# Kernel tuning notes

Measured on AMD Instinct MI355X. Metric: run time of the kernel, lower is better.

## Reference

```python
import jax, jax.numpy as jnp
import numpy as np

B, T, D, H, DH = 2, 2048, 1024, 16, 64
LN_EPS = 1e-5


def setup_inputs() -> dict:
    key = jax.random.key(0)
    ks = jax.random.split(key, 16)
    s = 0.02
    return {
        "query_sequences": jax.random.normal(ks[0], (B, T, D), jnp.float32),
        "key_sequences": jax.random.normal(ks[1], (B, T, D), jnp.float32),
        "value_sequences": jax.random.normal(ks[2], (B, T, D), jnp.float32),
        "key_value_sequence_lengths": jax.random.randint(ks[3], (B,), 1, T + 1),
        "Wq": jax.random.normal(ks[4], (D, H * DH), jnp.float32) * s,
        "bq": jnp.zeros((H * DH,), jnp.float32),
        "Wk": jax.random.normal(ks[5], (D, H * DH), jnp.float32) * s,
        "bk": jnp.zeros((H * DH,), jnp.float32),
        "Wv": jax.random.normal(ks[6], (D, H * DH), jnp.float32) * s,
        "bv": jnp.zeros((H * DH,), jnp.float32),
        "Wo": jax.random.normal(ks[7], (H * DH, D), jnp.float32) * s,
        "bo": jnp.zeros((D,), jnp.float32),
        "gamma": jnp.ones((D,), jnp.float32),
        "beta": jnp.zeros((D,), jnp.float32),
    }


def _layer_norm(x, gamma, beta):
    mu = jnp.mean(x, axis=-1, keepdims=True)
    var = jnp.var(x, axis=-1, keepdims=True)
    return (x - mu) * jax.lax.rsqrt(var + LN_EPS) * gamma + beta


def reference(query_sequences, key_sequences, value_sequences,
              key_value_sequence_lengths, Wq, bq, Wk, bk, Wv, bv, Wo, bo,
              gamma, beta):
    # pre-LN (self-attn: same LN applied to q, k, v inputs)
    q_in = _layer_norm(query_sequences, gamma, beta)
    k_in = _layer_norm(key_sequences, gamma, beta)
    v_in = _layer_norm(value_sequences, gamma, beta)

    # projections -> [B, H, T, DH]
    q = (q_in @ Wq + bq).reshape(B, T, H, DH).transpose(0, 2, 1, 3)
    k = (k_in @ Wk + bk).reshape(B, T, H, DH).transpose(0, 2, 1, 3)
    v = (v_in @ Wv + bv).reshape(B, T, H, DH).transpose(0, 2, 1, 3)

    scale = 1.0 / jnp.sqrt(jnp.float32(DH))
    scores = jnp.einsum('bhtd,bhTd->bhtT', q, k) * scale  # [B,H,Tq,Tk]

    # key padding mask: key position < sequence length
    pad_mask = jnp.arange(T)[None, None, None, :] < key_value_sequence_lengths[:, None, None, None]
    # causal mask (self_attn and in_decoder)
    causal = jnp.tril(jnp.ones((T, T), bool))[None, None]
    mask = pad_mask & causal
    scores = jnp.where(mask, scores, -jnp.inf)

    attn = jax.nn.softmax(scores, axis=-1)  # dropout=0 (eval)
    attn_viz = attn.reshape(B * H, T, T)

    out = jnp.einsum('bhtT,bhTd->bhtd', attn, v)
    out = out.transpose(0, 2, 1, 3).reshape(B, T, H * DH)
    out = out @ Wo + bo
    return out, attn_viz
```

## Files before the change

kernel.cpp:

```cpp
#include <hip/hip_runtime.h>
#include <hip/hip_bf16.h>

#define B_  2
#define T_  2048
#define D_  1024
#define H_  16
#define DH_ 64
#define M_  (B_*T_)

typedef __bf16 bf16;
typedef __bf16 bf16x8 __attribute__((ext_vector_type(8)));
typedef __bf16 bf16x4 __attribute__((ext_vector_type(4)));
typedef float  f32x4  __attribute__((ext_vector_type(4)));

__global__ __launch_bounds__(256) void ln_kernel(
    const float* __restrict__ xq, const float* __restrict__ xk,
    const float* __restrict__ xv, const float* __restrict__ gamma,
    const float* __restrict__ beta,
    bf16* __restrict__ oq, bf16* __restrict__ ok, bf16* __restrict__ ov)
{
    const int row = blockIdx.x;
    const int sel = blockIdx.y;
    const float* x = (sel == 0 ? xq : sel == 1 ? xk : xv) + (size_t)row * D_;
    bf16*        o = (sel == 0 ? oq : sel == 1 ? ok : ov) + (size_t)row * D_;
    const int tid = threadIdx.x;

    float4 v = *(const float4*)&x[tid * 4];
    float s  = v.x + v.y + v.z + v.w;
    float s2 = v.x*v.x + v.y*v.y + v.z*v.z + v.w*v.w;
    for (int off = 32; off > 0; off >>= 1) {
        s  += __shfl_down(s,  off, 64);
        s2 += __shfl_down(s2, off, 64);
    }
    __shared__ float red[8];
    const int wave = tid >> 6, lane = tid & 63;
    if (lane == 0) { red[wave] = s; red[4 + wave] = s2; }
    __syncthreads();
    s  = red[0] + red[1] + red[2] + red[3];
    s2 = red[4] + red[5] + red[6] + red[7];
    const float mu   = s * (1.0f / D_);
    const float var  = s2 * (1.0f / D_) - mu * mu;
    const float rstd = rsqrtf(var + 1e-5f);

    float4 g  = *(const float4*)&gamma[tid * 4];
    float4 bb = *(const float4*)&beta[tid * 4];
    bf16x4 o4;
    o4[0] = (bf16)((v.x - mu) * rstd * g.x + bb.x);
    o4[1] = (bf16)((v.y - mu) * rstd * g.y + bb.y);
    o4[2] = (bf16)((v.z - mu) * rstd * g.z + bb.z);
    o4[3] = (bf16)((v.w - mu) * rstd * g.w + bb.w);
    *(bf16x4*)&o[tid * 4] = o4;
}

__global__ __launch_bounds__(256) void wconv_kernel(
    const float* __restrict__ Wq, const float* __restrict__ Wk,
    const float* __restrict__ Wv, const float* __restrict__ Wo,
    bf16* __restrict__ wqt, bf16* __restrict__ wkt,
    bf16* __restrict__ wvt, bf16* __restrict__ wot)
{
    const float* Ws[4] = {Wq, Wk, Wv, Wo};
    bf16*        Wt[4] = {wqt, wkt, wvt, wot};
    const float* W = Ws[blockIdx.z];
    bf16*        O = Wt[blockIdx.z];
    const int n0 = blockIdx.x * 32, k0 = blockIdx.y * 32;
    __shared__ float tile[32][33];
    const int tid = threadIdx.x;
    #pragma unroll
    for (int i = 0; i < 4; i++) {
        int e = tid + i * 256;
        int r = e >> 5, c = e & 31;
        tile[r][c] = W[(size_t)(k0 + r) * 1024 + n0 + c];
    }
    __syncthreads();
    #pragma unroll
    for (int i = 0; i < 4; i++) {
        int e = tid + i * 256;
        int nr = e >> 5, kc = e & 31;
        O[(size_t)(n0 + nr) * 1024 + k0 + kc] = (bf16)tile[kc][nr];
    }
}

template <int MODE>
__global__ __launch_bounds__(256) void gemm_bt(
    const bf16* __restrict__ A, const bf16* __restrict__ Bt,
    const float* __restrict__ bias, void* __restrict__ Cout)
{
    __shared__ bf16 sA[128][40];
    __shared__ bf16 sB[128][40];
    const int tid  = threadIdx.x;
    const int wave = tid >> 6, lane = tid & 63;
    const int quad = lane >> 4, l16 = lane & 15;
    const int wr = (wave >> 1) * 64, wc = (wave & 1) * 64;
    const int m0 = blockIdx.y * 128, n0 = blockIdx.x * 128;

    f32x4 acc[4][4] = {};
    const int r0   = tid >> 2;
    const int r1   = 64 + (tid >> 2);
    const int off0 = (tid & 3) * 8;

    for (int k0 = 0; k0 < 1024; k0 += 32) {
        __syncthreads();
        *(bf16x8*)&sA[r0][off0] = *(const bf16x8*)&A[(size_t)(m0 + r0) * 1024 + k0 + off0];
        *(bf16x8*)&sA[r1][off0] = *(const bf16x8*)&A[(size_t)(m0 + r1) * 1024 + k0 + off0];
        *(bf16x8*)&sB[r0][off0] = *(const bf16x8*)&Bt[(size_t)(n0 + r0) * 1024 + k0 + off0];
        *(bf16x8*)&sB[r1][off0] = *(const bf16x8*)&Bt[(size_t)(n0 + r1) * 1024 + k0 + off0];
        __syncthreads();

        bf16x8 af[4], bfr[4];
        #pragma unroll
        for (int i = 0; i < 4; i++) af[i]  = *(bf16x8*)&sA[wr + i * 16 + l16][quad * 8];
        #pragma unroll
        for (int j = 0; j < 4; j++) bfr[j] = *(bf16x8*)&sB[wc + j * 16 + l16][quad * 8];
        #pragma unroll
        for (int i = 0; i < 4; i++)
            #pragma unroll
            for (int j = 0; j < 4; j++)
                acc[i][j] = __builtin_amdgcn_mfma_f32_16x16x32_bf16(af[i], bfr[j], acc[i][j], 0, 0, 0);
    }

    #pragma unroll
    for (int i = 0; i < 4; i++) {
        #pragma unroll
        for (int j = 0; j < 4; j++) {
            const int n = n0 + wc + j * 16 + l16;
            const float bia = bias[n];
            #pragma unroll
            for (int r = 0; r < 4; r++) {
                const int m = m0 + wr + i * 16 + quad * 4 + r;
                const float v = acc[i][j][r] + bia;
                if (MODE == 0) {
                    const int b = m >> 11, t = m & 2047, h = n >> 6, dh = n & 63;
                    ((bf16*)Cout)[(((size_t)b * H_ + h) * T_ + t) * DH_ + dh] = (bf16)v;
                } else {
                    ((float*)Cout)[(size_t)m * 1024 + n] = v;
                }
            }
        }
    }
}

__global__ __launch_bounds__(256) void attn_kernel(
    const bf16* __restrict__ Qh, const bf16* __restrict__ Kh,
    const bf16* __restrict__ Vh, const int* __restrict__ lens,
    float* __restrict__ attn_out, bf16* __restrict__ Obuf)
{
    const int bh = blockIdx.y;
    const int b = bh >> 4, h = bh & 15;
    const int bx = blockIdx.x;
    const int q0 = bx * 64;
    const int len = lens[b];
    const bf16* Qp = Qh + (size_t)bh * T_ * DH_;
    const bf16* Kp = Kh + (size_t)bh * T_ * DH_;
    const bf16* Vp = Vh + (size_t)bh * T_ * DH_;
    float* attnp = attn_out + (size_t)bh * T_ * T_;

    const int tid  = threadIdx.x;
    const int wave = tid >> 6, lane = tid & 63;
    const int quad = lane >> 4, l16 = lane & 15;
    const float scale = 0.125f;

    __shared__ bf16 Kt[64][72];
    __shared__ bf16 Vt[64][72];
    __shared__ bf16 Pt[4][16][72];

    const int qrow = q0 + wave * 16 + l16;
    const bf16x8 aq0 = *(const bf16x8*)&Qp[(size_t)qrow * DH_ + quad * 8];
    const bf16x8 aq1 = *(const bf16x8*)&Qp[(size_t)qrow * DH_ + 32 + quad * 8];

    const int jb_hi = min(bx, (len - 1) >> 6);

    const int krow0 = tid >> 3;
    const int krow1 = 32 + (tid >> 3);
    const int koff0 = (tid & 7) * 8;

    float mrow[4], lrow[4];
    #pragma unroll
    for (int r = 0; r < 4; r++) { mrow[r] = -INFINITY; lrow[r] = 0.0f; }

    for (int jb = 0; jb <= jb_hi; jb++) {
        __syncthreads();
        *(bf16x8*)&Kt[krow0][koff0] = *(const bf16x8*)&Kp[(size_t)(jb * 64 + krow0) * DH_ + koff0];
        *(bf16x8*)&Kt[krow1][koff0] = *(const bf16x8*)&Kp[(size_t)(jb * 64 + krow1) * DH_ + koff0];
        __syncthreads();

        f32x4 sc[4];
        #pragma unroll
        for (int c = 0; c < 4; c++) {
            bf16x8 b0 = *(bf16x8*)&Kt[c * 16 + l16][quad * 8];
            bf16x8 b1 = *(bf16x8*)&Kt[c * 16 + l16][32 + quad * 8];
            f32x4 s = {};
            s = __builtin_amdgcn_mfma_f32_16x16x32_bf16(aq0, b0, s, 0, 0, 0);
            s = __builtin_amdgcn_mfma_f32_16x16x32_bf16(aq1, b1, s, 0, 0, 0);
            sc[c] = s;
        }
        #pragma unroll
        for (int r = 0; r < 4; r++) {
            const int t_g = q0 + wave * 16 + quad * 4 + r;
            float sv[4];
            float tmax = -INFINITY;
            #pragma unroll
            for (int c = 0; c < 4; c++) {
                const int k_g = jb * 64 + c * 16 + l16;
                const bool valid = (k_g <= t_g) && (k_g < len);
                sv[c] = valid ? sc[c][r] * scale : -INFINITY;
                tmax = fmaxf(tmax, sv[c]);
            }
            #pragma unroll
            for (int o = 1; o < 16; o <<= 1) tmax = fmaxf(tmax, __shfl_xor(tmax, o, 16));
            const float newm = fmaxf(mrow[r], tmax);
            float psum = 0.0f;
            #pragma unroll
            for (int c = 0; c < 4; c++) psum += __expf(sv[c] - newm);
            #pragma unroll
            for (int o = 1; o < 16; o <<= 1) psum += __shfl_xor(psum, o, 16);
            lrow[r] = lrow[r] * __expf(mrow[r] - newm) + psum;
            mrow[r] = newm;
        }
    }

    float linv[4];
    #pragma unroll
    for (int r = 0; r < 4; r++) linv[r] = 1.0f / lrow[r];

    f32x4 oacc[4] = {};
    for (int jb = 0; jb <= jb_hi; jb++) {
        __syncthreads();
        *(bf16x8*)&Kt[krow0][koff0] = *(const bf16x8*)&Kp[(size_t)(jb * 64 + krow0) * DH_ + koff0];
        *(bf16x8*)&Kt[krow1][koff0] = *(const bf16x8*)&Kp[(size_t)(jb * 64 + krow1) * DH_ + koff0];
        {
            bf16x8 v0 = *(const bf16x8*)&Vp[(size_t)(jb * 64 + krow0) * DH_ + koff0];
            bf16x8 v1 = *(const bf16x8*)&Vp[(size_t)(jb * 64 + krow1) * DH_ + koff0];
            #pragma unroll
            for (int j2 = 0; j2 < 8; j2++) {
                Vt[koff0 + j2][krow0] = v0[j2];
                Vt[koff0 + j2][krow1] = v1[j2];
            }
        }
        __syncthreads();

        f32x4 sc[4];
        #pragma unroll
        for (int c = 0; c < 4; c++) {
            bf16x8 b0 = *(bf16x8*)&Kt[c * 16 + l16][quad * 8];
            bf16x8 b1 = *(bf16x8*)&Kt[c * 16 + l16][32 + quad * 8];
            f32x4 s = {};
            s = __builtin_amdgcn_mfma_f32_16x16x32_bf16(aq0, b0, s, 0, 0, 0);
            s = __builtin_amdgcn_mfma_f32_16x16x32_bf16(aq1, b1, s, 0, 0, 0);
            sc[c] = s;
        }
        #pragma unroll
        for (int c = 0; c < 4; c++) {
            const int k_g = jb * 64 + c * 16 + l16;
            #pragma unroll
            for (int r = 0; r < 4; r++) {
                const int t_g = q0 + wave * 16 + quad * 4 + r;
                const bool valid = (k_g <= t_g) && (k_g < len);
                const float p = valid ? __expf(sc[c][r] * scale - mrow[r]) * linv[r] : 0.0f;
                attnp[(size_t)t_g * T_ + k_g] = p;
                Pt[wave][quad * 4 + r][c * 16 + l16] = (bf16)p;
            }
        }
        asm volatile("s_waitcnt lgkmcnt(0)" ::: "memory");
        #pragma unroll
        for (int ks = 0; ks < 2; ks++) {
            bf16x8 ap = *(bf16x8*)&Pt[wave][l16][ks * 32 + quad * 8];
            #pragma unroll
            for (int c = 0; c < 4; c++) {
                bf16x8 vb = *(bf16x8*)&Vt[c * 16 + l16][ks * 32 + quad * 8];
                oacc[c] = __builtin_amdgcn_mfma_f32_16x16x32_bf16(ap, vb, oacc[c], 0, 0, 0);
            }
        }
    }

    const int zc0 = (jb_hi + 1) * 64;
    if (zc0 < T_) {
        const int span4 = (T_ - zc0) >> 2;
        for (int r = 0; r < 16; r++) {
            const size_t rowbase = (size_t)(q0 + wave * 16 + r) * T_ + zc0;
            for (int c4 = lane; c4 < span4; c4 += 64) {
                *(float4*)&attnp[rowbase + (size_t)c4 * 4] = make_float4(0.f, 0.f, 0.f, 0.f);
            }
        }
    }

    #pragma unroll
    for (int c = 0; c < 4; c++) {
        #pragma unroll
        for (int r = 0; r < 4; r++) {
            const int t_g = q0 + wave * 16 + quad * 4 + r;
            const int dh = c * 16 + l16;
            Obuf[(size_t)(b * T_ + t_g) * 1024 + h * DH_ + dh] = (bf16)oacc[c][r];
        }
    }
}

extern "C" void kernel_launch(void* const* d_in, const int* in_sizes, int n_in,
                              void* d_out, int out_size, void* d_ws, size_t ws_size,
                              hipStream_t stream)
{
    const float* xq    = (const float*)d_in[0];
    const float* xk    = (const float*)d_in[1];
    const float* xv    = (const float*)d_in[2];
    const int*   lens  = (const int*)d_in[3];
    const float* Wq    = (const float*)d_in[4];
    const float* bq    = (const float*)d_in[5];
    const float* Wk    = (const float*)d_in[6];
    const float* bk    = (const float*)d_in[7];
    const float* Wv    = (const float*)d_in[8];
    const float* bv    = (const float*)d_in[9];
    const float* Wo    = (const float*)d_in[10];
    const float* bo    = (const float*)d_in[11];
    const float* gamma = (const float*)d_in[12];
    const float* beta  = (const float*)d_in[13];

    float* out      = (float*)d_out;
    float* attn_out = out + (size_t)M_ * D_;

    char* ws = (char*)d_ws;
    bf16* lnq  = (bf16*)ws; ws += (size_t)M_ * D_ * 2;
    bf16* lnk  = (bf16*)ws; ws += (size_t)M_ * D_ * 2;
    bf16* lnv  = (bf16*)ws; ws += (size_t)M_ * D_ * 2;
    bf16* wqt  = (bf16*)ws; ws += (size_t)1024 * 1024 * 2;
    bf16* wkt  = (bf16*)ws; ws += (size_t)1024 * 1024 * 2;
    bf16* wvt  = (bf16*)ws; ws += (size_t)1024 * 1024 * 2;
    bf16* wot  = (bf16*)ws; ws += (size_t)1024 * 1024 * 2;
    bf16* Qh   = (bf16*)ws; ws += (size_t)M_ * D_ * 2;
    bf16* Kh   = (bf16*)ws; ws += (size_t)M_ * D_ * 2;
    bf16* Vh   = (bf16*)ws; ws += (size_t)M_ * D_ * 2;
    bf16* Obuf = (bf16*)ws; ws += (size_t)M_ * D_ * 2;

    ln_kernel<<<dim3(M_, 3), 256, 0, stream>>>(xq, xk, xv, gamma, beta, lnq, lnk, lnv);
    wconv_kernel<<<dim3(32, 32, 4), 256, 0, stream>>>(Wq, Wk, Wv, Wo, wqt, wkt, wvt, wot);
    gemm_bt<0><<<dim3(8, 32), 256, 0, stream>>>(lnq, wqt, bq, (void*)Qh);
    gemm_bt<0><<<dim3(8, 32), 256, 0, stream>>>(lnk, wkt, bk, (void*)Kh);
    gemm_bt<0><<<dim3(8, 32), 256, 0, stream>>>(lnv, wvt, bv, (void*)Vh);
    attn_kernel<<<dim3(T_ / 64, B_ * H_), 256, 0, stream>>>(Qh, Kh, Vh, lens, attn_out, Obuf);
    gemm_bt<1><<<dim3(8, 32), 256, 0, stream>>>(Obuf, wot, bo, (void*)out);
}
```

Baseline: 777.8 us.

## Drop online max in attention, pretranspose V, coalesce attn writes, direct-to-LDS GEMM loads

A new kernel writes V transposed once, into the dead lnq buffer. The attention kernel can then read K and V fragments straight from global memory, with no LDS staging and no block barriers. The first pass now sums exp2 of the scaled scores without subtracting a running max, and unmasked tiles take a fast path that skips mask checks. Probabilities are staged in fp32 LDS so each tile of the attention matrix is written with coalesced float4 stores. The projection GEMM switches to global_load_lds 16-byte loads into unpadded shared tiles. Skipping the max subtraction assumes scores stay small enough not to overflow exp, and removing the padding may add LDS bank conflicts.

```diff
diff --git a/kernel.cpp b/kernel.cpp
--- a/kernel.cpp
+++ b/kernel.cpp
@@ -12,6 +12,12 @@
 typedef __bf16 bf16x8 __attribute__((ext_vector_type(8)));
 typedef __bf16 bf16x4 __attribute__((ext_vector_type(4)));
 typedef float  f32x4  __attribute__((ext_vector_type(4)));
+
+#define SCL2 0.18033688011112042f
+
+#define GLD16(g, l) __builtin_amdgcn_global_load_lds( \
+    (const __attribute__((address_space(1))) void*)(g), \
+    (__attribute__((address_space(3))) void*)(l), 16, 0, 0)
 
 __global__ __launch_bounds__(256) void ln_kernel(
     const float* __restrict__ xq, const float* __restrict__ xk,
@@ -80,13 +86,32 @@
     }
 }
 
+__global__ __launch_bounds__(256) void vtrans_kernel(
+    const bf16* __restrict__ Vh, bf16* __restrict__ VhT)
+{
+    const int bh = blockIdx.y, t0 = blockIdx.x * 64;
+    const bf16* src = Vh  + (size_t)bh * T_ * DH_;
+    bf16*       dst = VhT + (size_t)bh * T_ * DH_;
+    __shared__ bf16 tile[64][72];
+    const int tid = threadIdx.x;
+    const int r = tid >> 3, c8 = (tid & 7) * 8;
+    *(bf16x8*)&tile[r][c8]      = *(const bf16x8*)&src[(size_t)(t0 + r) * DH_ + c8];
+    *(bf16x8*)&tile[32 + r][c8] = *(const bf16x8*)&src[(size_t)(t0 + 32 + r) * DH_ + c8];
+    __syncthreads();
+    bf16x8 o0, o1;
+    #pragma unroll
+    for (int j = 0; j < 8; j++) { o0[j] = tile[c8 + j][r]; o1[j] = tile[c8 + j][32 + r]; }
+    *(bf16x8*)&dst[(size_t)r * T_ + t0 + c8]        = o0;
+    *(bf16x8*)&dst[(size_t)(32 + r) * T_ + t0 + c8] = o1;
+}
+
 template <int MODE>
 __global__ __launch_bounds__(256) void gemm_bt(
     const bf16* __restrict__ A, const bf16* __restrict__ Bt,
     const float* __restrict__ bias, void* __restrict__ Cout)
 {
-    __shared__ bf16 sA[128][40];
-    __shared__ bf16 sB[128][40];
+    __shared__ bf16 sA[128][32];
+    __shared__ bf16 sB[128][32];
     const int tid  = threadIdx.x;
     const int wave = tid >> 6, lane = tid & 63;
     const int quad = lane >> 4, l16 = lane & 15;
@@ -94,16 +119,24 @@
     const int m0 = blockIdx.y * 128, n0 = blockIdx.x * 128;
 
     f32x4 acc[4][4] = {};
-    const int r0   = tid >> 2;
-    const int r1   = 64 + (tid >> 2);
-    const int off0 = (tid & 3) * 8;
+
+    const int srow = wave * 32 + (lane >> 2);
+    const int scol = (lane & 3) * 8;
+    const bf16* gA0 = &A [(size_t)(m0 + srow)      * 1024 + scol];
+    const bf16* gA1 = &A [(size_t)(m0 + srow + 16) * 1024 + scol];
+    const bf16* gB0 = &Bt[(size_t)(n0 + srow)      * 1024 + scol];
+    const bf16* gB1 = &Bt[(size_t)(n0 + srow + 16) * 1024 + scol];
+    bf16* lA0 = &sA[wave * 32][0];
+    bf16* lA1 = &sA[wave * 32 + 16][0];
+    bf16* lB0 = &sB[wave * 32][0];
+    bf16* lB1 = &sB[wave * 32 + 16][0];
 
     for (int k0 = 0; k0 < 1024; k0 += 32) {
         __syncthreads();
-        *(bf16x8*)&sA[r0][off0] = *(const bf16x8*)&A[(size_t)(m0 + r0) * 1024 + k0 + off0];
-        *(bf16x8*)&sA[r1][off0] = *(const bf16x8*)&A[(size_t)(m0 + r1) * 1024 + k0 + off0];
-        *(bf16x8*)&sB[r0][off0] = *(const bf16x8*)&Bt[(size_t)(n0 + r0) * 1024 + k0 + off0];
-        *(bf16x8*)&sB[r1][off0] = *(const bf16x8*)&Bt[(size_t)(n0 + r1) * 1024 + k0 + off0];
+        GLD16(gA0 + k0, lA0);
+        GLD16(gA1 + k0, lA1);
+        GLD16(gB0 + k0, lB0);
+        GLD16(gB1 + k0, lB1);
         __syncthreads();
 
         bf16x8 af[4], bfr[4];
@@ -141,7 +174,7 @@
 
 __global__ __launch_bounds__(256) void attn_kernel(
     const bf16* __restrict__ Qh, const bf16* __restrict__ Kh,
-    const bf16* __restrict__ Vh, const int* __restrict__ lens,
+    const bf16* __restrict__ VhT, const int* __restrict__ lens,
     float* __restrict__ attn_out, bf16* __restrict__ Obuf)
 {
     const int bh = blockIdx.y;
@@ -149,19 +182,16 @@
     const int bx = blockIdx.x;
     const int q0 = bx * 64;
     const int len = lens[b];
-    const bf16* Qp = Qh + (size_t)bh * T_ * DH_;
-    const bf16* Kp = Kh + (size_t)bh * T_ * DH_;
-    const bf16* Vp = Vh + (size_t)bh * T_ * DH_;
+    const bf16* Qp = Qh  + (size_t)bh * T_ * DH_;
+    const bf16* Kp = Kh  + (size_t)bh * T_ * DH_;
+    const bf16* Vp = VhT + (size_t)bh * T_ * DH_;
     float* attnp = attn_out + (size_t)bh * T_ * T_;
 
     const int tid  = threadIdx.x;
     const int wave = tid >> 6, lane = tid & 63;
     const int quad = lane >> 4, l16 = lane & 15;
-    const float scale = 0.125f;
-
-    __shared__ bf16 Kt[64][72];
-    __shared__ bf16 Vt[64][72];
-    __shared__ bf16 Pt[4][16][72];
+
+    __shared__ float Pf[4][16][68];
 
     const int qrow = q0 + wave * 16 + l16;
     const bf16x8 aq0 = *(const bf16x8*)&Qp[(size_t)qrow * DH_ + quad * 8];
@@ -169,106 +199,97 @@
 
     const int jb_hi = min(bx, (len - 1) >> 6);
 
-    const int krow0 = tid >> 3;
-    const int krow1 = 32 + (tid >> 3);
-    const int koff0 = (tid & 7) * 8;
-
-    float mrow[4], lrow[4];
-    #pragma unroll
-    for (int r = 0; r < 4; r++) { mrow[r] = -INFINITY; lrow[r] = 0.0f; }
+    float lsum[4] = {0.f, 0.f, 0.f, 0.f};
 
     for (int jb = 0; jb <= jb_hi; jb++) {
-        __syncthreads();
-        *(bf16x8*)&Kt[krow0][koff0] = *(const bf16x8*)&Kp[(size_t)(jb * 64 + krow0) * DH_ + koff0];
-        *(bf16x8*)&Kt[krow1][koff0] = *(const bf16x8*)&Kp[(size_t)(jb * 64 + krow1) * DH_ + koff0];
-        __syncthreads();
-
         f32x4 sc[4];
         #pragma unroll
         for (int c = 0; c < 4; c++) {
-            bf16x8 b0 = *(bf16x8*)&Kt[c * 16 + l16][quad * 8];
-            bf16x8 b1 = *(bf16x8*)&Kt[c * 16 + l16][32 + quad * 8];
+            const size_t krow = (size_t)(jb * 64 + c * 16 + l16) * DH_;
+            bf16x8 b0 = *(const bf16x8*)&Kp[krow + quad * 8];
+            bf16x8 b1 = *(const bf16x8*)&Kp[krow + 32 + quad * 8];
             f32x4 s = {};
             s = __builtin_amdgcn_mfma_f32_16x16x32_bf16(aq0, b0, s, 0, 0, 0);
             s = __builtin_amdgcn_mfma_f32_16x16x32_bf16(aq1, b1, s, 0, 0, 0);
             sc[c] = s;
         }
-        #pragma unroll
-        for (int r = 0; r < 4; r++) {
-            const int t_g = q0 + wave * 16 + quad * 4 + r;
-            float sv[4];
-            float tmax = -INFINITY;
+        if ((jb < bx) && ((jb + 1) * 64 <= len)) {
+            #pragma unroll
+            for (int c = 0; c < 4; c++)
+                #pragma unroll
+                for (int r = 0; r < 4; r++)
+                    lsum[r] += __builtin_amdgcn_exp2f(sc[c][r] * SCL2);
+        } else {
             #pragma unroll
             for (int c = 0; c < 4; c++) {
                 const int k_g = jb * 64 + c * 16 + l16;
-                const bool valid = (k_g <= t_g) && (k_g < len);
-                sv[c] = valid ? sc[c][r] * scale : -INFINITY;
-                tmax = fmaxf(tmax, sv[c]);
-            }
-            #pragma unroll
-            for (int o = 1; o < 16; o <<= 1) tmax = fmaxf(tmax, __shfl_xor(tmax, o, 16));
-            const float newm = fmaxf(mrow[r], tmax);
-            float psum = 0.0f;
-            #pragma unroll
-            for (int c = 0; c < 4; c++) psum += __expf(sv[c] - newm);
-            #pragma unroll
-            for (int o = 1; o < 16; o <<= 1) psum += __shfl_xor(psum, o, 16);
-            lrow[r] = lrow[r] * __expf(mrow[r] - newm) + psum;
-            mrow[r] = newm;
-        }
-    }
-
+                #pragma unroll
+                for (int r = 0; r < 4; r++) {
+                    const int t_g = q0 + wave * 16 + quad * 4 + r;
+                    const bool valid = (k_g <= t_g) & (k_g < len);
+                    lsum[r] += valid ? __builtin_amdgcn_exp2f(sc[c][r] * SCL2) : 0.0f;
+                }
+            }
+        }
+    }
     float linv[4];
     #pragma unroll
-    for (int r = 0; r < 4; r++) linv[r] = 1.0f / lrow[r];
+    for (int r = 0; r < 4; r++) {
+        float v = lsum[r];
+        #pragma unroll
+        for (int o = 1; o < 16; o <<= 1) v += __shfl_xor(v, o, 16);
+        linv[r] = 1.0f / v;
+    }
 
     f32x4 oacc[4] = {};
     for (int jb = 0; jb <= jb_hi; jb++) {
-        __syncthreads();
-        *(bf16x8*)&Kt[krow0][koff0] = *(const bf16x8*)&Kp[(size_t)(jb * 64 + krow0) * DH_ + koff0];
-        *(bf16x8*)&Kt[krow1][koff0] = *(const bf16x8*)&Kp[(size_t)(jb * 64 + krow1) * DH_ + koff0];
-        {
-            bf16x8 v0 = *(const bf16x8*)&Vp[(size_t)(jb * 64 + krow0) * DH_ + koff0];
-            bf16x8 v1 = *(const bf16x8*)&Vp[(size_t)(jb * 64 + krow1) * DH_ + koff0];
-            #pragma unroll
-            for (int j2 = 0; j2 < 8; j2++) {
-                Vt[koff0 + j2][krow0] = v0[j2];
-                Vt[koff0 + j2][krow1] = v1[j2];
-            }
-        }
-        __syncthreads();
-
         f32x4 sc[4];
         #pragma unroll
         for (int c = 0; c < 4; c++) {
-            bf16x8 b0 = *(bf16x8*)&Kt[c * 16 + l16][quad * 8];
-            bf16x8 b1 = *(bf16x8*)&Kt[c * 16 + l16][32 + quad * 8];
+            const size_t krow = (size_t)(jb * 64 + c * 16 + l16) * DH_;
+            bf16x8 b0 = *(const bf16x8*)&Kp[krow + quad * 8];
+            bf16x8 b1 = *(const bf16x8*)&Kp[krow + 32 + quad * 8];
             f32x4 s = {};
             s = __builtin_amdgcn_mfma_f32_16x16x32_bf16(aq0, b0, s, 0, 0, 0);
             s = __builtin_amdgcn_mfma_f32_16x16x32_bf16(aq1, b1, s, 0, 0, 0);
             sc[c] = s;
         }
+        const bool fullt = (jb < bx) && ((jb + 1) * 64 <= len);
         #pragma unroll
         for (int c = 0; c < 4; c++) {
             const int k_g = jb * 64 + c * 16 + l16;
             #pragma unroll
             for (int r = 0; r < 4; r++) {
-                const int t_g = q0 + wave * 16 + quad * 4 + r;
-                const bool valid = (k_g <= t_g) && (k_g < len);
-                const float p = valid ? __expf(sc[c][r] * scale - mrow[r]) * linv[r] : 0.0f;
-                attnp[(size_t)t_g * T_ + k_g] = p;
-                Pt[wave][quad * 4 + r][c * 16 + l16] = (bf16)p;
+                float p = __builtin_amdgcn_exp2f(sc[c][r] * SCL2) * linv[r];
+                if (!fullt) {
+                    const int t_g = q0 + wave * 16 + quad * 4 + r;
+                    if (!((k_g <= t_g) & (k_g < len))) p = 0.0f;
+                }
+                Pf[wave][quad * 4 + r][c * 16 + l16] = p;
             }
         }
         asm volatile("s_waitcnt lgkmcnt(0)" ::: "memory");
+
         #pragma unroll
         for (int ks = 0; ks < 2; ks++) {
-            bf16x8 ap = *(bf16x8*)&Pt[wave][l16][ks * 32 + quad * 8];
+            f32x4 p0 = *(f32x4*)&Pf[wave][l16][ks * 32 + quad * 8];
+            f32x4 p1 = *(f32x4*)&Pf[wave][l16][ks * 32 + quad * 8 + 4];
+            bf16x8 ap;
+            ap[0] = (bf16)p0[0]; ap[1] = (bf16)p0[1]; ap[2] = (bf16)p0[2]; ap[3] = (bf16)p0[3];
+            ap[4] = (bf16)p1[0]; ap[5] = (bf16)p1[1]; ap[6] = (bf16)p1[2]; ap[7] = (bf16)p1[3];
             #pragma unroll
             for (int c = 0; c < 4; c++) {
-                bf16x8 vb = *(bf16x8*)&Vt[c * 16 + l16][ks * 32 + quad * 8];
+                const bf16x8 vb = *(const bf16x8*)&Vp[(size_t)(c * 16 + l16) * T_ + jb * 64 + ks * 32 + quad * 8];
                 oacc[c] = __builtin_amdgcn_mfma_f32_16x16x32_bf16(ap, vb, oacc[c], 0, 0, 0);
             }
+        }
+
+        #pragma unroll
+        for (int s = 0; s < 4; s++) {
+            const int row = s * 4 + (lane >> 4);
+            const int c4  = (lane & 15) * 4;
+            f32x4 v4 = *(f32x4*)&Pf[wave][row][c4];
+            *(f32x4*)&attnp[(size_t)(q0 + wave * 16 + row) * T_ + jb * 64 + c4] = v4;
         }
     }
 
@@ -328,12 +349,14 @@
     bf16* Kh   = (bf16*)ws; ws += (size_t)M_ * D_ * 2;
     bf16* Vh   = (bf16*)ws; ws += (size_t)M_ * D_ * 2;
     bf16* Obuf = (bf16*)ws; ws += (size_t)M_ * D_ * 2;
+    bf16* VhT  = lnq;
 
     ln_kernel<<<dim3(M_, 3), 256, 0, stream>>>(xq, xk, xv, gamma, beta, lnq, lnk, lnv);
     wconv_kernel<<<dim3(32, 32, 4), 256, 0, stream>>>(Wq, Wk, Wv, Wo, wqt, wkt, wvt, wot);
     gemm_bt<0><<<dim3(8, 32), 256, 0, stream>>>(lnq, wqt, bq, (void*)Qh);
     gemm_bt<0><<<dim3(8, 32), 256, 0, stream>>>(lnk, wkt, bk, (void*)Kh);
     gemm_bt<0><<<dim3(8, 32), 256, 0, stream>>>(lnv, wvt, bv, (void*)Vh);
-    attn_kernel<<<dim3(T_ / 64, B_ * H_), 256, 0, stream>>>(Qh, Kh, Vh, lens, attn_out, Obuf);
+    vtrans_kernel<<<dim3(T_ / 64, B_ * H_), 256, 0, stream>>>(Vh, VhT);
+    attn_kernel<<<dim3(T_ / 64, B_ * H_), 256, 0, stream>>>(Qh, Kh, VhT, lens, attn_out, Obuf);
     gemm_bt<1><<<dim3(8, 32), 256, 0, stream>>>(Obuf, wot, bo, (void*)out);
 }
```

Result: slower. 856.8 us (+10.2%).
